# Performance work log

Measured on AMD Instinct MI355X. Metric: run time of the kernel, lower is better.

## Reference

```python
import jax, jax.numpy as jnp
import numpy as np

B, C, M, H, W = 4, 12, 2, 320, 320
TOL = 1e-6
MAX_ITER = 10


def to_c(t):
    # [..., 2] real -> complex
    return jax.lax.complex(t[..., 0], t[..., 1])


def to_r(t):
    return jnp.stack([jnp.real(t), jnp.imag(t)], axis=-1)


def fft2c(x):
    return jnp.fft.fft2(x, axes=(-2, -1), norm='ortho')


def ifft2c(x):
    return jnp.fft.ifft2(x, axes=(-2, -1), norm='ortho')


def A_op(x, sm, mk):
    # x: [B,M,H,W] complex, sm: [B,C,M,H,W] complex, mk: [B,C,H,W] real
    coil_imgs = jnp.sum(x[:, None] * sm, axis=2)  # [B,C,H,W]
    return fft2c(coil_imgs) * mk


def AT_op(y, sm, mk):
    img = ifft2c(y * mk)  # [B,C,H,W]
    return jnp.sum(jnp.conj(sm) * img[:, :, None], axis=1)  # [B,M,H,W]


def cg_solve(x0, Mop, tol=TOL, max_iter=MAX_ITER):
    b = x0.shape[0]
    x0x0 = jnp.sum(jnp.abs(x0.reshape(b, -1)) ** 2, axis=-1)  # [B] real

    def body(carry, _):
        x, r, p, rr = carry
        active = jnp.min(rr / x0x0) > tol  # tol check, gated like the while-loop
        q = Mop(p)
        pq = jnp.sum((p * jnp.conj(q)).reshape(b, -1), axis=-1)  # complexDot(p, q)
        alpha = rr.astype(x0.dtype) / pq  # complex_div(rr, <p,q>)
        a = alpha[:, None, None, None]
        x_new = x + a * p
        r_new = r - a * q
        rr_new = jnp.sum(jnp.abs(r_new.reshape(b, -1)) ** 2, axis=-1)
        beta = (rr_new / rr)[:, None, None, None].astype(x0.dtype)
        p_new = r_new + beta * p
        new = (x_new, r_new, p_new, rr_new)
        carry = jax.tree.map(lambda n, o: jnp.where(active, n, o), new, carry)
        return carry, None

    rr0 = jnp.sum(jnp.abs(x0.reshape(b, -1)) ** 2, axis=-1)
    init = (jnp.zeros_like(x0), x0, x0, rr0)
    (x, _, _, _), _ = jax.lax.scan(body, init, None, length=max_iter)
    return x


def setup_inputs() -> dict:
    key = jax.random.key(0)
    k1, k2, k3, k4 = jax.random.split(key, 4)
    x = jax.random.normal(k1, (B, M, H, W, 2), dtype=jnp.float32)
    y = jax.random.normal(k2, (B, C, H, W, 2), dtype=jnp.float32)
    smaps = jax.random.normal(k3, (B, C, M, H, W, 2), dtype=jnp.float32) * 0.2
    mask = jax.random.randint(k4, (B, C, H, W, 1), 0, 2).astype(jnp.float32)
    lambda_a = jnp.full((1,), 0.05, dtype=jnp.float32)
    return {"x": x, "y": y, "smaps": smaps, "mask": mask, "lambda_a": lambda_a}


def reference(x, y, smaps, mask, lambda_a):
    z = to_c(x)          # [B,M,H,W]
    yc = to_c(y)         # [B,C,H,W]
    sm = to_c(smaps)     # [B,C,M,H,W]
    mk = mask[..., 0]    # [B,C,H,W]
    lam = lambda_a[0]

    x0 = lam * AT_op(yc, sm, mk) + z

    def Mop(p):
        return lam * AT_op(A_op(p, sm, mk), sm, mk) + p

    return to_r(cg_solve(x0, Mop))
```

## Files before the change

kernel.cpp:

```cpp
#include <hip/hip_runtime.h>
#include <math.h>

#define NB 4
#define NC 12
#define NM 2
#define NN 320
#define NHW (NN*NN)
#define NBC (NB*NC)
#define CG_TOL 1e-6f
#define NITER 10
#define CBLK 400

#define TWO_PI_F 6.28318530717958647692f

typedef float2 c32;

__device__ __forceinline__ c32 cmul(c32 a, c32 b){ return make_float2(a.x*b.x - a.y*b.y, a.x*b.y + a.y*b.x); }
__device__ __forceinline__ c32 cmulj(c32 a, c32 b){ return make_float2(a.x*b.x + a.y*b.y, a.x*b.y - a.y*b.x); }
__device__ __forceinline__ c32 cadd(c32 a, c32 b){ return make_float2(a.x+b.x, a.y+b.y); }
__device__ __forceinline__ c32 csub(c32 a, c32 b){ return make_float2(a.x-b.x, a.y-b.y); }
__device__ __forceinline__ c32 cscale(c32 a, float s){ return make_float2(a.x*s, a.y*s); }

__device__ __forceinline__ float wave_reduce_f(float v) {
  #pragma unroll
  for (int off = 32; off >= 1; off >>= 1) v += __shfl_xor(v, off, 64);
  return v;
}
__device__ __forceinline__ c32 wave_reduce_c(c32 v) {
  #pragma unroll
  for (int off = 32; off >= 1; off >>= 1) {
    v.x += __shfl_xor(v.x, off, 64);
    v.y += __shfl_xor(v.y, off, 64);
  }
  return v;
}

__global__ __launch_bounds__(256)
void twiddle_init(c32* __restrict__ T320, c32* __restrict__ T64)
{
  const int t = threadIdx.x;
  {
    float s, c; sincosf(TWO_PI_F * (float)t / 320.f, &s, &c);
    T320[t] = make_float2(c, s);
  }
  if (t < 32) {
    float s, c; sincosf(TWO_PI_F * (float)t / 64.f, &s, &c);
    T64[t] = make_float2(c, s);
  }
}

template<int DIR>
__device__ __forceinline__ void fft320_tw(c32 A[5], const c32 ct[4], const c32 tw[6], int lane)
{
  constexpr float C72  = 0.30901699437494745f, S72  = 0.9510565162951535f;
  constexpr float C144 = -0.8090169943749475f, S144 = 0.5877852522924731f;
  const float sgn = (float)DIR;
  const c32 w51 = make_float2(C72,  sgn*S72);
  const c32 w52 = make_float2(C144, sgn*S144);
  const c32 w53 = make_float2(C144, -sgn*S144);
  const c32 w54 = make_float2(C72,  -sgn*S72);
  c32 v0=A[0], v1=A[1], v2=A[2], v3=A[3], v4=A[4];
  A[0] = cadd(cadd(v0, v1), cadd(cadd(v2, v3), v4));
  A[1] = cadd(v0, cadd(cadd(cmul(v1,w51), cmul(v2,w52)), cadd(cmul(v3,w53), cmul(v4,w54))));
  A[2] = cadd(v0, cadd(cadd(cmul(v1,w52), cmul(v2,w54)), cadd(cmul(v3,w51), cmul(v4,w53))));
  A[3] = cadd(v0, cadd(cadd(cmul(v1,w53), cmul(v2,w51)), cadd(cmul(v3,w54), cmul(v4,w52))));
  A[4] = cadd(v0, cadd(cadd(cmul(v1,w54), cmul(v2,w53)), cadd(cmul(v3,w52), cmul(v4,w51))));
  A[1] = cmul(A[1], ct[0]);
  A[2] = cmul(A[2], ct[1]);
  A[3] = cmul(A[3], ct[2]);
  A[4] = cmul(A[4], ct[3]);
  #pragma unroll
  for (int s = 0; s < 6; ++s) {
    const int m = 32 >> s;
    const c32 w = tw[s];
    const bool up = (lane & m) != 0;
    #pragma unroll
    for (int k1 = 0; k1 < 5; ++k1) {
      c32 o;
      o.x = __shfl_xor(A[k1].x, m, 64);
      o.y = __shfl_xor(A[k1].y, m, 64);
      c32 lo = cadd(A[k1], o);
      c32 hi = cmul(csub(o, A[k1]), w);
      A[k1] = up ? hi : lo;
    }
  }
}

template<int DIR, int IN_MODE, int OUT_MODE>
__global__ __launch_bounds__(256)
void fft_pass(const c32* __restrict__ in, c32* __restrict__ out,
              const c32* __restrict__ pvec, const c32* __restrict__ smaps,
              const float* __restrict__ mask, const float* __restrict__ flag,
              const c32* __restrict__ T320, const c32* __restrict__ T64)
{
  if (flag != nullptr && flag[0] == 0.f) return;
  __shared__ c32 tile[8][NN + 2];
  const int tid  = threadIdx.x;
  const int lane = tid & 63;
  const int wv   = tid >> 6;
  const int bc   = blockIdx.y;
  const int r0   = blockIdx.x * 8;
  const float sgn = (float)DIR;

  c32 ct[4], tw[6];
  #pragma unroll
  for (int k = 0; k < 4; ++k) {
    c32 t = T320[(k + 1) * lane];
    ct[k] = make_float2(t.x, sgn * t.y);
  }
  #pragma unroll
  for (int s = 0; s < 6; ++s) {
    const int m = 32 >> s;
    c32 t = T64[(lane & (m - 1)) << s];
    tw[s] = make_float2(t.x, sgn * t.y);
  }
  const int rv6 = __brev((unsigned)lane) >> 26;

  #pragma unroll
  for (int rep = 0; rep < 2; ++rep) {
    const int ri  = wv * 2 + rep;
    const int row = r0 + ri;
    c32 A[5];
    if constexpr (IN_MODE == 0) {
      #pragma unroll
      for (int j = 0; j < 5; ++j)
        A[j] = in[((size_t)bc * NN + row) * NN + lane + 64*j];
    } else if constexpr (IN_MODE == 1) {
      const int b = bc / NC;
      const int c = bc % NC;
      #pragma unroll
      for (int j = 0; j < 5; ++j) {
        const int col = lane + 64*j;
        const size_t hw = (size_t)row * NN + col;
        c32 p0 = pvec[(size_t)(b*NM + 0) * NHW + hw];
        c32 p1 = pvec[(size_t)(b*NM + 1) * NHW + hw];
        c32 s0 = smaps[(size_t)((b*NC + c)*NM + 0) * NHW + hw];
        c32 s1 = smaps[(size_t)((b*NC + c)*NM + 1) * NHW + hw];
        A[j] = cadd(cmul(p0, s0), cmul(p1, s1));
      }
    } else {
      #pragma unroll
      for (int j = 0; j < 5; ++j) {
        const size_t idx = ((size_t)bc * NN + row) * NN + lane + 64*j;
        A[j] = cscale(in[idx], mask[idx]);
      }
    }
    fft320_tw<DIR>(A, ct, tw, lane);
    #pragma unroll
    for (int k1 = 0; k1 < 5; ++k1)
      tile[ri][k1 + 5*rv6] = A[k1];
  }
  __syncthreads();
  if constexpr (OUT_MODE != 2) {
    #pragma unroll
    for (int it = 0; it < 10; ++it) {
      const int idx = it * 256 + tid;
      const int u = idx >> 3;
      const int d = idx & 7;
      c32 val = tile[d][u];
      const size_t oidx = ((size_t)bc * NN + u) * NN + (r0 + d);
      if constexpr (OUT_MODE == 1) val = cscale(val, mask[oidx]);
      out[oidx] = val;
    }
  } else {
    #pragma unroll
    for (int it = 0; it < 10; ++it) {
      const int idx = it * 256 + tid;
      const int d = idx / NN;
      const int u = idx - d * NN;
      out[((size_t)bc * NN + (r0 + d)) * NN + u] = tile[d][u];
    }
  }
}

__global__ __launch_bounds__(256)
void fft_mask_ifft(const c32* __restrict__ in, c32* __restrict__ out,
                   const float* __restrict__ mask, const float* __restrict__ flag,
                   const c32* __restrict__ T320, const c32* __restrict__ T64)
{
  if (flag[0] == 0.f) return;
  __shared__ c32 tile[8][NN + 2];
  const int tid  = threadIdx.x;
  const int lane = tid & 63;
  const int wv   = tid >> 6;
  const int bc   = blockIdx.y;
  const int r0   = blockIdx.x * 8;

  c32 ctf[4], twf[6], cti[4], twi[6];
  #pragma unroll
  for (int k = 0; k < 4; ++k) {
    c32 t = T320[(k + 1) * lane];
    ctf[k] = make_float2(t.x, -t.y);
    cti[k] = make_float2(t.x,  t.y);
  }
  #pragma unroll
  for (int s = 0; s < 6; ++s) {
    const int m = 32 >> s;
    c32 t = T64[(lane & (m - 1)) << s];
    twf[s] = make_float2(t.x, -t.y);
    twi[s] = make_float2(t.x,  t.y);
  }
  const int rv6 = __brev((unsigned)lane) >> 26;

  #pragma unroll
  for (int rep = 0; rep < 2; ++rep) {
    const int ri  = wv * 2 + rep;
    const int row = r0 + ri;
    c32 A[5];
    #pragma unroll
    for (int j = 0; j < 5; ++j)
      A[j] = in[((size_t)bc * NN + row) * NN + lane + 64*j];
    fft320_tw<-1>(A, ctf, twf, lane);
    #pragma unroll
    for (int k1 = 0; k1 < 5; ++k1) {
      const int kh = k1 + 5*rv6;
      A[k1] = cscale(A[k1], mask[(size_t)bc * NHW + (size_t)kh * NN + row]);
    }
    #pragma unroll
    for (int k1 = 0; k1 < 5; ++k1)
      tile[ri][k1 + 5*rv6] = A[k1];
    c32 Bv[5];
    #pragma unroll
    for (int j = 0; j < 5; ++j)
      Bv[j] = tile[ri][lane + 64*j];
    fft320_tw<1>(Bv, cti, twi, lane);
    #pragma unroll
    for (int k1 = 0; k1 < 5; ++k1)
      tile[ri][k1 + 5*rv6] = Bv[k1];
  }
  __syncthreads();
  #pragma unroll
  for (int it = 0; it < 10; ++it) {
    const int idx = it * 256 + tid;
    const int u = idx >> 3;
    const int d = idx & 7;
    out[((size_t)bc * NN + u) * NN + (r0 + d)] = tile[d][u];
  }
}

__global__ __launch_bounds__(256)
void init_combine(const c32* __restrict__ img, const c32* __restrict__ smaps,
                  const c32* __restrict__ z, c32* __restrict__ x,
                  c32* __restrict__ r, c32* __restrict__ p,
                  const float* __restrict__ lam, float* __restrict__ part)
{
  const int b  = blockIdx.y;
  const int hw = blockIdx.x * 256 + threadIdx.x;
  const float l0 = lam[0] * (1.f / (float)NN);
  c32 a0 = make_float2(0.f,0.f), a1 = make_float2(0.f,0.f);
  #pragma unroll
  for (int c = 0; c < NC; ++c) {
    c32 iv = img[(size_t)(b*NC + c) * NHW + hw];
    c32 s0 = smaps[(size_t)((b*NC + c)*NM + 0) * NHW + hw];
    c32 s1 = smaps[(size_t)((b*NC + c)*NM + 1) * NHW + hw];
    a0 = cadd(a0, cmulj(s0, iv));
    a1 = cadd(a1, cmulj(s1, iv));
  }
  const size_t i0 = (size_t)(b*NM + 0) * NHW + hw;
  const size_t i1 = (size_t)(b*NM + 1) * NHW + hw;
  c32 x00 = cadd(cscale(a0, l0), z[i0]);
  c32 x01 = cadd(cscale(a1, l0), z[i1]);
  x[i0] = make_float2(0.f,0.f); x[i1] = make_float2(0.f,0.f);
  r[i0] = x00; r[i1] = x01;
  p[i0] = x00; p[i1] = x01;
  float acc = x00.x*x00.x + x00.y*x00.y + x01.x*x01.x + x01.y*x01.y;
  acc = wave_reduce_f(acc);
  __shared__ float sred[4];
  const int lane = threadIdx.x & 63, wv = threadIdx.x >> 6;
  if (lane == 0) sred[wv] = acc;
  __syncthreads();
  if (threadIdx.x == 0) part[b*CBLK + blockIdx.x] = sred[0]+sred[1]+sred[2]+sred[3];
}

__global__ void reduce_init(const float* __restrict__ part, float* __restrict__ x0x0,
                            float* __restrict__ rr0, float* __restrict__ flags)
{
  const int lane = threadIdx.x & 63;
  const int b = threadIdx.x >> 6;
  float s = 0.f;
  for (int j = lane; j < CBLK; j += 64) s += part[b*CBLK + j];
  s = wave_reduce_f(s);
  if (lane == 0) { x0x0[b] = s; rr0[b] = s; }
  if (threadIdx.x == 0) flags[0] = 1.f;
}

__global__ __launch_bounds__(256)
void q_combine(const c32* __restrict__ img, const c32* __restrict__ smaps,
               const c32* __restrict__ p, c32* __restrict__ q,
               const float* __restrict__ lam, const float* __restrict__ flag,
               c32* __restrict__ pqpart)
{
  if (flag[0] == 0.f) return;
  const int b  = blockIdx.y;
  const int hw = blockIdx.x * 256 + threadIdx.x;
  const float lq = lam[0] * (1.f / (float)NHW);
  c32 a0 = make_float2(0.f,0.f), a1 = make_float2(0.f,0.f);
  #pragma unroll
  for (int c = 0; c < NC; ++c) {
    c32 iv = img[(size_t)(b*NC + c) * NHW + hw];
    c32 s0 = smaps[(size_t)((b*NC + c)*NM + 0) * NHW + hw];
    c32 s1 = smaps[(size_t)((b*NC + c)*NM + 1) * NHW + hw];
    a0 = cadd(a0, cmulj(s0, iv));
    a1 = cadd(a1, cmulj(s1, iv));
  }
  const size_t i0 = (size_t)(b*NM + 0) * NHW + hw;
  const size_t i1 = (size_t)(b*NM + 1) * NHW + hw;
  c32 p0 = p[i0], p1 = p[i1];
  c32 q0 = cadd(cscale(a0, lq), p0);
  c32 q1 = cadd(cscale(a1, lq), p1);
  q[i0] = q0; q[i1] = q1;
  c32 s = cadd(cmulj(q0, p0), cmulj(q1, p1));
  s = wave_reduce_c(s);
  __shared__ c32 sred[4];
  const int lane = threadIdx.x & 63, wv = threadIdx.x >> 6;
  if (lane == 0) sred[wv] = s;
  __syncthreads();
  if (threadIdx.x == 0)
    pqpart[b*CBLK + blockIdx.x] = cadd(cadd(sred[0], sred[1]), cadd(sred[2], sred[3]));
}

__global__ void reduce_pq(const c32* __restrict__ pqpart, c32* __restrict__ pqout,
                          const float* __restrict__ flag)
{
  if (flag[0] == 0.f) return;
  const int lane = threadIdx.x & 63;
  const int b = threadIdx.x >> 6;
  c32 s = make_float2(0.f, 0.f);
  for (int j = lane; j < CBLK; j += 64) s = cadd(s, pqpart[b*CBLK + j]);
  s = wave_reduce_c(s);
  if (lane == 0) pqout[b] = s;
}

__global__ __launch_bounds__(256)
void update1(c32* __restrict__ x, c32* __restrict__ r,
             const c32* __restrict__ p, const c32* __restrict__ q,
             const float* __restrict__ rr_i, const c32* __restrict__ pq_i,
             const float* __restrict__ flag, float* __restrict__ part)
{
  if (flag[0] == 0.f) return;
  const int b  = blockIdx.y;
  const int hw = blockIdx.x * 256 + threadIdx.x;
  const float rrv = rr_i[b];
  const c32 pqv = pq_i[b];
  const float den = pqv.x*pqv.x + pqv.y*pqv.y;
  const c32 alpha = make_float2(rrv * pqv.x / den, -rrv * pqv.y / den);
  float acc = 0.f;
  #pragma unroll
  for (int m = 0; m < NM; ++m) {
    const size_t idx = (size_t)(b*NM + m) * NHW + hw;
    c32 pe = p[idx], qe = q[idx];
    c32 xe = cadd(x[idx], cmul(alpha, pe));
    c32 re = csub(r[idx], cmul(alpha, qe));
    x[idx] = xe; r[idx] = re;
    acc += re.x*re.x + re.y*re.y;
  }
  acc = wave_reduce_f(acc);
  __shared__ float sred[4];
  const int lane = threadIdx.x & 63, wv = threadIdx.x >> 6;
  if (lane == 0) sred[wv] = acc;
  __syncthreads();
  if (threadIdx.x == 0) part[b*CBLK + blockIdx.x] = sred[0]+sred[1]+sred[2]+sred[3];
}

__global__ void reduce_rr(const float* __restrict__ part, const float* __restrict__ rr_i,
                          float* __restrict__ rr_n, const float* __restrict__ x0x0,
                          const float* __restrict__ flag_i, float* __restrict__ flag_n)
{
  const int lane = threadIdx.x & 63;
  const int b = threadIdx.x >> 6;
  __shared__ float sred[4];
  __shared__ float sx0[4];
  if (flag_i[0] == 0.f) {
    if (lane == 0) rr_n[b] = rr_i[b];
    if (threadIdx.x == 0) flag_n[0] = 0.f;
    return;
  }
  float s = 0.f;
  for (int j = lane; j < CBLK; j += 64) s += part[b*CBLK + j];
  s = wave_reduce_f(s);
  if (lane == 0) { rr_n[b] = s; sred[b] = s; sx0[b] = x0x0[b]; }
  __syncthreads();
  if (threadIdx.x == 0) {
    float mn = 1e30f;
    #pragma unroll
    for (int bb = 0; bb < NB; ++bb) mn = fminf(mn, sred[bb] / sx0[bb]);
    flag_n[0] = (mn > CG_TOL) ? 1.f : 0.f;
  }
}

__global__ __launch_bounds__(256)
void update2(c32* __restrict__ p, const c32* __restrict__ r,
             const float* __restrict__ rr_i, const float* __restrict__ rr_n,
             const float* __restrict__ flag)
{
  if (flag[0] == 0.f) return;
  const int b  = blockIdx.y;
  const int hw = blockIdx.x * 256 + threadIdx.x;
  const float beta = rr_n[b] / rr_i[b];
  #pragma unroll
  for (int m = 0; m < NM; ++m) {
    const size_t idx = (size_t)(b*NM + m) * NHW + hw;
    p[idx] = cadd(r[idx], cscale(p[idx], beta));
  }
}

extern "C" void kernel_launch(void* const* d_in, const int* in_sizes, int n_in,
                              void* d_out, int out_size, void* d_ws, size_t ws_size,
                              hipStream_t stream)
{
  const c32*  z   = (const c32*)d_in[0];
  const c32*  y   = (const c32*)d_in[1];
  const c32*  sm  = (const c32*)d_in[2];
  const float* mk = (const float*)d_in[3];
  const float* lam= (const float*)d_in[4];
  c32* x = (c32*)d_out;

  char* base = (char*)d_ws;
  size_t off = 0;
  auto walloc = [&](size_t bytes) -> void* {
    void* ptr = base + off;
    off += (bytes + 255) & ~(size_t)255;
    return ptr;
  };
  c32* buf1   = (c32*)walloc((size_t)NBC * NHW * sizeof(c32));
  c32* buf2   = (c32*)walloc((size_t)NBC * NHW * sizeof(c32));
  c32* rv     = (c32*)walloc((size_t)NB * NM * NHW * sizeof(c32));
  c32* pv     = (c32*)walloc((size_t)NB * NM * NHW * sizeof(c32));
  c32* qv     = (c32*)walloc((size_t)NB * NM * NHW * sizeof(c32));
  c32* pqpart = (c32*)walloc((size_t)NB * CBLK * sizeof(c32));
  c32* pq     = (c32*)walloc((size_t)NITER * NB * sizeof(c32));
  float* x0x0 = (float*)walloc(NB * sizeof(float));
  float* rr   = (float*)walloc((NITER + 1) * NB * sizeof(float));
  float* flags= (float*)walloc((NITER + 1) * sizeof(float));
  float* part1= (float*)walloc((size_t)NB * CBLK * sizeof(float));
  c32* T320   = (c32*)walloc(256 * sizeof(c32));
  c32* T64    = (c32*)walloc(32 * sizeof(c32));
  (void)ws_size; (void)in_sizes; (void)n_in; (void)out_size;

  dim3 fgrid(NN / 8, NBC), blk(256);
  dim3 cgrid(CBLK, NB);

  twiddle_init<<<1, 256, 0, stream>>>(T320, T64);

  fft_pass<1, 2, 0><<<fgrid, blk, 0, stream>>>(y,    buf2, nullptr, nullptr, mk,      nullptr, T320, T64);
  fft_pass<1, 0, 0><<<fgrid, blk, 0, stream>>>(buf2, buf1, nullptr, nullptr, nullptr, nullptr, T320, T64);
  init_combine<<<cgrid, blk, 0, stream>>>(buf1, sm, z, x, rv, pv, lam, part1);
  reduce_init<<<1, 256, 0, stream>>>(part1, x0x0, rr, flags);

  for (int i = 0; i < NITER; ++i) {
    const float* fl = flags + i;
    fft_pass<-1, 1, 0><<<fgrid, blk, 0, stream>>>(nullptr, buf2, pv, sm, nullptr, fl, T320, T64);
    fft_mask_ifft<<<fgrid, blk, 0, stream>>>(buf2, buf1, mk, fl, T320, T64);
    fft_pass<1, 0, 2><<<fgrid, blk, 0, stream>>>(buf1, buf2, nullptr, nullptr, nullptr, fl, T320, T64);
    q_combine<<<cgrid, blk, 0, stream>>>(buf2, sm, pv, qv, lam, fl, pqpart);
    reduce_pq<<<1, 256, 0, stream>>>(pqpart, pq + i*NB, fl);
    update1<<<cgrid, blk, 0, stream>>>(x, rv, pv, qv, rr + i*NB, pq + i*NB, fl, part1);
    reduce_rr<<<1, 256, 0, stream>>>(part1, rr + i*NB, rr + (i+1)*NB, x0x0, fl, flags + (i+1));
    update2<<<cgrid, blk, 0, stream>>>(pv, rv, rr + i*NB, rr + (i+1)*NB, fl);
  }
}
```

Baseline: 430.8 us.

## Fuse p-update into first FFT pass, fold pq reduction, batch two-row FFTs

```diff
diff --git a/kernel.cpp b/kernel.cpp
--- a/kernel.cpp
+++ b/kernel.cpp
@@ -21,6 +21,12 @@
 __device__ __forceinline__ c32 csub(c32 a, c32 b){ return make_float2(a.x-b.x, a.y-b.y); }
 __device__ __forceinline__ c32 cscale(c32 a, float s){ return make_float2(a.x*s, a.y*s); }
 
+template<bool FWD>
+__device__ __forceinline__ c32 twmul(c32 a, c32 t){
+  return FWD ? make_float2(a.x*t.x + a.y*t.y, a.y*t.x - a.x*t.y)
+             : make_float2(a.x*t.x - a.y*t.y, a.y*t.x + a.x*t.y);
+}
+
 __device__ __forceinline__ float wave_reduce_f(float v) {
   #pragma unroll
   for (int off = 32; off >= 1; off >>= 1) v += __shfl_xor(v, off, 64);
@@ -49,127 +55,160 @@
   }
 }
 
-template<int DIR>
-__device__ __forceinline__ void fft320_tw(c32 A[5], const c32 ct[4], const c32 tw[6], int lane)
-{
-  constexpr float C72  = 0.30901699437494745f, S72  = 0.9510565162951535f;
-  constexpr float C144 = -0.8090169943749475f, S144 = 0.5877852522924731f;
-  const float sgn = (float)DIR;
-  const c32 w51 = make_float2(C72,  sgn*S72);
-  const c32 w52 = make_float2(C144, sgn*S144);
-  const c32 w53 = make_float2(C144, -sgn*S144);
-  const c32 w54 = make_float2(C72,  -sgn*S72);
-  c32 v0=A[0], v1=A[1], v2=A[2], v3=A[3], v4=A[4];
-  A[0] = cadd(cadd(v0, v1), cadd(cadd(v2, v3), v4));
-  A[1] = cadd(v0, cadd(cadd(cmul(v1,w51), cmul(v2,w52)), cadd(cmul(v3,w53), cmul(v4,w54))));
-  A[2] = cadd(v0, cadd(cadd(cmul(v1,w52), cmul(v2,w54)), cadd(cmul(v3,w51), cmul(v4,w53))));
-  A[3] = cadd(v0, cadd(cadd(cmul(v1,w53), cmul(v2,w51)), cadd(cmul(v3,w54), cmul(v4,w52))));
-  A[4] = cadd(v0, cadd(cadd(cmul(v1,w54), cmul(v2,w53)), cadd(cmul(v3,w52), cmul(v4,w51))));
-  A[1] = cmul(A[1], ct[0]);
-  A[2] = cmul(A[2], ct[1]);
-  A[3] = cmul(A[3], ct[2]);
-  A[4] = cmul(A[4], ct[3]);
+template<bool FWD>
+__device__ __forceinline__ void radix5(c32 V[5]) {
+  constexpr float C1 = 0.30901699437494745f;
+  constexpr float S1 = 0.9510565162951535f;
+  constexpr float C2 = -0.8090169943749475f;
+  constexpr float S2 = 0.5877852522924731f;
+  constexpr float sg = FWD ? -1.f : 1.f;
+  const c32 w1 = make_float2(C1,  sg*S1);
+  const c32 w2 = make_float2(C2,  sg*S2);
+  const c32 w3 = make_float2(C2, -sg*S2);
+  const c32 w4 = make_float2(C1, -sg*S1);
+  c32 v0=V[0], v1=V[1], v2=V[2], v3=V[3], v4=V[4];
+  V[0] = cadd(cadd(v0, v1), cadd(cadd(v2, v3), v4));
+  V[1] = cadd(v0, cadd(cadd(cmul(v1,w1), cmul(v2,w2)), cadd(cmul(v3,w3), cmul(v4,w4))));
+  V[2] = cadd(v0, cadd(cadd(cmul(v1,w2), cmul(v2,w4)), cadd(cmul(v3,w1), cmul(v4,w3))));
+  V[3] = cadd(v0, cadd(cadd(cmul(v1,w3), cmul(v2,w1)), cadd(cmul(v3,w4), cmul(v4,w2))));
+  V[4] = cadd(v0, cadd(cadd(cmul(v1,w4), cmul(v2,w3)), cadd(cmul(v3,w2), cmul(v4,w1))));
+}
+
+template<bool FWD>
+__device__ __forceinline__ void fft320_x2(c32 A[5], c32 B[5],
+                                          const c32 ct[4], const c32 tw[6], int lane)
+{
+  radix5<FWD>(A);
+  radix5<FWD>(B);
+  #pragma unroll
+  for (int k = 1; k < 5; ++k) {
+    A[k] = twmul<FWD>(A[k], ct[k-1]);
+    B[k] = twmul<FWD>(B[k], ct[k-1]);
+  }
   #pragma unroll
   for (int s = 0; s < 6; ++s) {
     const int m = 32 >> s;
     const c32 w = tw[s];
     const bool up = (lane & m) != 0;
-    #pragma unroll
-    for (int k1 = 0; k1 < 5; ++k1) {
-      c32 o;
-      o.x = __shfl_xor(A[k1].x, m, 64);
-      o.y = __shfl_xor(A[k1].y, m, 64);
-      c32 lo = cadd(A[k1], o);
-      c32 hi = cmul(csub(o, A[k1]), w);
-      A[k1] = up ? hi : lo;
+    c32 oA[5], oB[5];
+    #pragma unroll
+    for (int k = 0; k < 5; ++k) { oA[k].x = __shfl_xor(A[k].x, m, 64); oA[k].y = __shfl_xor(A[k].y, m, 64); }
+    #pragma unroll
+    for (int k = 0; k < 5; ++k) { oB[k].x = __shfl_xor(B[k].x, m, 64); oB[k].y = __shfl_xor(B[k].y, m, 64); }
+    #pragma unroll
+    for (int k = 0; k < 5; ++k) {
+      c32 loA = cadd(A[k], oA[k]);
+      c32 hiA = twmul<FWD>(csub(oA[k], A[k]), w);
+      A[k] = up ? hiA : loA;
+      c32 loB = cadd(B[k], oB[k]);
+      c32 hiB = twmul<FWD>(csub(oB[k], B[k]), w);
+      B[k] = up ? hiB : loB;
     }
   }
 }
 
-template<int DIR, int IN_MODE, int OUT_MODE>
+#define LOAD_TWIDDLES \
+  c32 ct[4], tw[6]; \
+  _Pragma("unroll") for (int k_ = 0; k_ < 4; ++k_) ct[k_] = T320[(k_ + 1) * lane]; \
+  _Pragma("unroll") for (int s_ = 0; s_ < 6; ++s_) tw[s_] = T64[(lane & ((32 >> s_) - 1)) << s_];
+
+template<bool FWD, bool MASK_IN, bool NAT_OUT>
 __global__ __launch_bounds__(256)
 void fft_pass(const c32* __restrict__ in, c32* __restrict__ out,
-              const c32* __restrict__ pvec, const c32* __restrict__ smaps,
               const float* __restrict__ mask, const float* __restrict__ flag,
               const c32* __restrict__ T320, const c32* __restrict__ T64)
 {
   if (flag != nullptr && flag[0] == 0.f) return;
   __shared__ c32 tile[8][NN + 2];
-  const int tid  = threadIdx.x;
-  const int lane = tid & 63;
-  const int wv   = tid >> 6;
-  const int bc   = blockIdx.y;
-  const int r0   = blockIdx.x * 8;
-  const float sgn = (float)DIR;
-
-  c32 ct[4], tw[6];
-  #pragma unroll
-  for (int k = 0; k < 4; ++k) {
-    c32 t = T320[(k + 1) * lane];
-    ct[k] = make_float2(t.x, sgn * t.y);
-  }
-  #pragma unroll
-  for (int s = 0; s < 6; ++s) {
-    const int m = 32 >> s;
-    c32 t = T64[(lane & (m - 1)) << s];
-    tw[s] = make_float2(t.x, sgn * t.y);
-  }
+  const int tid = threadIdx.x, lane = tid & 63, wv = tid >> 6;
+  const int bc = blockIdx.y, r0 = blockIdx.x * 8;
+  LOAD_TWIDDLES
   const int rv6 = __brev((unsigned)lane) >> 26;
-
-  #pragma unroll
-  for (int rep = 0; rep < 2; ++rep) {
-    const int ri  = wv * 2 + rep;
-    const int row = r0 + ri;
-    c32 A[5];
-    if constexpr (IN_MODE == 0) {
-      #pragma unroll
-      for (int j = 0; j < 5; ++j)
-        A[j] = in[((size_t)bc * NN + row) * NN + lane + 64*j];
-    } else if constexpr (IN_MODE == 1) {
-      const int b = bc / NC;
-      const int c = bc % NC;
-      #pragma unroll
-      for (int j = 0; j < 5; ++j) {
-        const int col = lane + 64*j;
-        const size_t hw = (size_t)row * NN + col;
-        c32 p0 = pvec[(size_t)(b*NM + 0) * NHW + hw];
-        c32 p1 = pvec[(size_t)(b*NM + 1) * NHW + hw];
-        c32 s0 = smaps[(size_t)((b*NC + c)*NM + 0) * NHW + hw];
-        c32 s1 = smaps[(size_t)((b*NC + c)*NM + 1) * NHW + hw];
-        A[j] = cadd(cmul(p0, s0), cmul(p1, s1));
+  const int rA = r0 + wv*2, rB = rA + 1;
+  c32 A[5], B[5];
+  #pragma unroll
+  for (int j = 0; j < 5; ++j) {
+    const size_t iA = ((size_t)bc * NN + rA) * NN + lane + 64*j;
+    const size_t iB = ((size_t)bc * NN + rB) * NN + lane + 64*j;
+    A[j] = in[iA]; B[j] = in[iB];
+    if constexpr (MASK_IN) { A[j] = cscale(A[j], mask[iA]); B[j] = cscale(B[j], mask[iB]); }
+  }
+  fft320_x2<FWD>(A, B, ct, tw, lane);
+  #pragma unroll
+  for (int k = 0; k < 5; ++k) {
+    tile[wv*2    ][k + 5*rv6] = A[k];
+    tile[wv*2 + 1][k + 5*rv6] = B[k];
+  }
+  __syncthreads();
+  if constexpr (!NAT_OUT) {
+    #pragma unroll
+    for (int it = 0; it < 10; ++it) {
+      const int idx = it * 256 + tid, u = idx >> 3, d = idx & 7;
+      out[((size_t)bc * NN + u) * NN + (r0 + d)] = tile[d][u];
+    }
+  } else {
+    #pragma unroll
+    for (int it = 0; it < 10; ++it) {
+      const int idx = it * 256 + tid, d = idx / NN, u = idx - d * NN;
+      out[((size_t)bc * NN + (r0 + d)) * NN + u] = tile[d][u];
+    }
+  }
+}
+
+__global__ __launch_bounds__(256)
+void fft_comb(c32* __restrict__ out, const c32* __restrict__ pin,
+              const c32* __restrict__ rres, c32* __restrict__ pout,
+              const c32* __restrict__ smaps,
+              const float* __restrict__ rr_prev, const float* __restrict__ rr_cur,
+              const float* __restrict__ flag,
+              const c32* __restrict__ T320, const c32* __restrict__ T64)
+{
+  if (flag[0] == 0.f) return;
+  __shared__ c32 tile[8][NN + 2];
+  const int tid = threadIdx.x, lane = tid & 63, wv = tid >> 6;
+  const int bc = blockIdx.y, r0 = blockIdx.x * 8;
+  const int b = bc / NC, c = bc - b * NC;
+  const bool upd = (rr_cur != nullptr);
+  const float beta = upd ? rr_cur[b] / rr_prev[b] : 0.f;
+  LOAD_TWIDDLES
+  const int rv6 = __brev((unsigned)lane) >> 26;
+  const int rA = r0 + wv*2, rB = rA + 1;
+  const size_t m0 = (size_t)(b*NM + 0) * NHW, m1 = (size_t)(b*NM + 1) * NHW;
+  const size_t s0o = (size_t)((b*NC + c)*NM + 0) * NHW, s1o = (size_t)((b*NC + c)*NM + 1) * NHW;
+  c32 A[5], B[5];
+  #pragma unroll
+  for (int j = 0; j < 5; ++j) {
+    const size_t hA = (size_t)rA * NN + lane + 64*j;
+    const size_t hB = (size_t)rB * NN + lane + 64*j;
+    c32 r0A = rres[m0 + hA], r1A = rres[m1 + hA];
+    c32 r0B = rres[m0 + hB], r1B = rres[m1 + hB];
+    c32 p0A, p1A, p0B, p1B;
+    if (upd) {
+      p0A = cadd(r0A, cscale(pin[m0 + hA], beta));
+      p1A = cadd(r1A, cscale(pin[m1 + hA], beta));
+      p0B = cadd(r0B, cscale(pin[m0 + hB], beta));
+      p1B = cadd(r1B, cscale(pin[m1 + hB], beta));
+      if (c == 0) {
+        pout[m0 + hA] = p0A; pout[m1 + hA] = p1A;
+        pout[m0 + hB] = p0B; pout[m1 + hB] = p1B;
       }
     } else {
-      #pragma unroll
-      for (int j = 0; j < 5; ++j) {
-        const size_t idx = ((size_t)bc * NN + row) * NN + lane + 64*j;
-        A[j] = cscale(in[idx], mask[idx]);
-      }
+      p0A = r0A; p1A = r1A; p0B = r0B; p1B = r1B;
     }
-    fft320_tw<DIR>(A, ct, tw, lane);
-    #pragma unroll
-    for (int k1 = 0; k1 < 5; ++k1)
-      tile[ri][k1 + 5*rv6] = A[k1];
-  }
-  __syncthreads();
-  if constexpr (OUT_MODE != 2) {
-    #pragma unroll
-    for (int it = 0; it < 10; ++it) {
-      const int idx = it * 256 + tid;
-      const int u = idx >> 3;
-      const int d = idx & 7;
-      c32 val = tile[d][u];
-      const size_t oidx = ((size_t)bc * NN + u) * NN + (r0 + d);
-      if constexpr (OUT_MODE == 1) val = cscale(val, mask[oidx]);
-      out[oidx] = val;
-    }
-  } else {
-    #pragma unroll
-    for (int it = 0; it < 10; ++it) {
-      const int idx = it * 256 + tid;
-      const int d = idx / NN;
-      const int u = idx - d * NN;
-      out[((size_t)bc * NN + (r0 + d)) * NN + u] = tile[d][u];
-    }
+    A[j] = cadd(cmul(p0A, smaps[s0o + hA]), cmul(p1A, smaps[s1o + hA]));
+    B[j] = cadd(cmul(p0B, smaps[s0o + hB]), cmul(p1B, smaps[s1o + hB]));
+  }
+  fft320_x2<true>(A, B, ct, tw, lane);
+  #pragma unroll
+  for (int k = 0; k < 5; ++k) {
+    tile[wv*2    ][k + 5*rv6] = A[k];
+    tile[wv*2 + 1][k + 5*rv6] = B[k];
+  }
+  __syncthreads();
+  #pragma unroll
+  for (int it = 0; it < 10; ++it) {
+    const int idx = it * 256 + tid, u = idx >> 3, d = idx & 7;
+    out[((size_t)bc * NN + u) * NN + (r0 + d)] = tile[d][u];
   }
 }
 
@@ -180,60 +219,44 @@
 {
   if (flag[0] == 0.f) return;
   __shared__ c32 tile[8][NN + 2];
-  const int tid  = threadIdx.x;
-  const int lane = tid & 63;
-  const int wv   = tid >> 6;
-  const int bc   = blockIdx.y;
-  const int r0   = blockIdx.x * 8;
-
-  c32 ctf[4], twf[6], cti[4], twi[6];
-  #pragma unroll
-  for (int k = 0; k < 4; ++k) {
-    c32 t = T320[(k + 1) * lane];
-    ctf[k] = make_float2(t.x, -t.y);
-    cti[k] = make_float2(t.x,  t.y);
-  }
-  #pragma unroll
-  for (int s = 0; s < 6; ++s) {
-    const int m = 32 >> s;
-    c32 t = T64[(lane & (m - 1)) << s];
-    twf[s] = make_float2(t.x, -t.y);
-    twi[s] = make_float2(t.x,  t.y);
-  }
+  const int tid = threadIdx.x, lane = tid & 63, wv = tid >> 6;
+  const int bc = blockIdx.y, r0 = blockIdx.x * 8;
+  LOAD_TWIDDLES
   const int rv6 = __brev((unsigned)lane) >> 26;
-
-  #pragma unroll
-  for (int rep = 0; rep < 2; ++rep) {
-    const int ri  = wv * 2 + rep;
-    const int row = r0 + ri;
-    c32 A[5];
-    #pragma unroll
-    for (int j = 0; j < 5; ++j)
-      A[j] = in[((size_t)bc * NN + row) * NN + lane + 64*j];
-    fft320_tw<-1>(A, ctf, twf, lane);
-    #pragma unroll
-    for (int k1 = 0; k1 < 5; ++k1) {
-      const int kh = k1 + 5*rv6;
-      A[k1] = cscale(A[k1], mask[(size_t)bc * NHW + (size_t)kh * NN + row]);
-    }
-    #pragma unroll
-    for (int k1 = 0; k1 < 5; ++k1)
-      tile[ri][k1 + 5*rv6] = A[k1];
-    c32 Bv[5];
-    #pragma unroll
-    for (int j = 0; j < 5; ++j)
-      Bv[j] = tile[ri][lane + 64*j];
-    fft320_tw<1>(Bv, cti, twi, lane);
-    #pragma unroll
-    for (int k1 = 0; k1 < 5; ++k1)
-      tile[ri][k1 + 5*rv6] = Bv[k1];
+  const int rA = r0 + wv*2, rB = rA + 1;
+  c32 A[5], B[5];
+  #pragma unroll
+  for (int j = 0; j < 5; ++j) {
+    A[j] = in[((size_t)bc * NN + rA) * NN + lane + 64*j];
+    B[j] = in[((size_t)bc * NN + rB) * NN + lane + 64*j];
+  }
+  fft320_x2<true>(A, B, ct, tw, lane);
+  #pragma unroll
+  for (int k = 0; k < 5; ++k) {
+    const int kh = k + 5*rv6;
+    A[k] = cscale(A[k], mask[(size_t)bc * NHW + (size_t)kh * NN + rA]);
+    B[k] = cscale(B[k], mask[(size_t)bc * NHW + (size_t)kh * NN + rB]);
+  }
+  #pragma unroll
+  for (int k = 0; k < 5; ++k) {
+    tile[wv*2    ][k + 5*rv6] = A[k];
+    tile[wv*2 + 1][k + 5*rv6] = B[k];
+  }
+  #pragma unroll
+  for (int j = 0; j < 5; ++j) {
+    A[j] = tile[wv*2    ][lane + 64*j];
+    B[j] = tile[wv*2 + 1][lane + 64*j];
+  }
+  fft320_x2<false>(A, B, ct, tw, lane);
+  #pragma unroll
+  for (int k = 0; k < 5; ++k) {
+    tile[wv*2    ][k + 5*rv6] = A[k];
+    tile[wv*2 + 1][k + 5*rv6] = B[k];
   }
   __syncthreads();
   #pragma unroll
   for (int it = 0; it < 10; ++it) {
-    const int idx = it * 256 + tid;
-    const int u = idx >> 3;
-    const int d = idx & 7;
+    const int idx = it * 256 + tid, u = idx >> 3, d = idx & 7;
     out[((size_t)bc * NN + u) * NN + (r0 + d)] = tile[d][u];
   }
 }
@@ -319,31 +342,27 @@
     pqpart[b*CBLK + blockIdx.x] = cadd(cadd(sred[0], sred[1]), cadd(sred[2], sred[3]));
 }
 
-__global__ void reduce_pq(const c32* __restrict__ pqpart, c32* __restrict__ pqout,
-                          const float* __restrict__ flag)
-{
-  if (flag[0] == 0.f) return;
-  const int lane = threadIdx.x & 63;
-  const int b = threadIdx.x >> 6;
-  c32 s = make_float2(0.f, 0.f);
-  for (int j = lane; j < CBLK; j += 64) s = cadd(s, pqpart[b*CBLK + j]);
-  s = wave_reduce_c(s);
-  if (lane == 0) pqout[b] = s;
-}
-
 __global__ __launch_bounds__(256)
 void update1(c32* __restrict__ x, c32* __restrict__ r,
              const c32* __restrict__ p, const c32* __restrict__ q,
-             const float* __restrict__ rr_i, const c32* __restrict__ pq_i,
+             const float* __restrict__ rr_i, const c32* __restrict__ pqpart,
              const float* __restrict__ flag, float* __restrict__ part)
 {
   if (flag[0] == 0.f) return;
-  const int b  = blockIdx.y;
-  const int hw = blockIdx.x * 256 + threadIdx.x;
+  const int b = blockIdx.y;
+  const int t = threadIdx.x;
+  c32 s = make_float2(0.f, 0.f);
+  for (int j = t; j < CBLK; j += 256) s = cadd(s, pqpart[b*CBLK + j]);
+  s = wave_reduce_c(s);
+  __shared__ c32 spq[4];
+  const int lane = t & 63, wv = t >> 6;
+  if (lane == 0) spq[wv] = s;
+  __syncthreads();
+  const c32 pqv = cadd(cadd(spq[0], spq[1]), cadd(spq[2], spq[3]));
   const float rrv = rr_i[b];
-  const c32 pqv = pq_i[b];
   const float den = pqv.x*pqv.x + pqv.y*pqv.y;
   const c32 alpha = make_float2(rrv * pqv.x / den, -rrv * pqv.y / den);
+  const int hw = blockIdx.x * 256 + t;
   float acc = 0.f;
   #pragma unroll
   for (int m = 0; m < NM; ++m) {
@@ -356,10 +375,9 @@
   }
   acc = wave_reduce_f(acc);
   __shared__ float sred[4];
-  const int lane = threadIdx.x & 63, wv = threadIdx.x >> 6;
   if (lane == 0) sred[wv] = acc;
   __syncthreads();
-  if (threadIdx.x == 0) part[b*CBLK + blockIdx.x] = sred[0]+sred[1]+sred[2]+sred[3];
+  if (t == 0) part[b*CBLK + blockIdx.x] = sred[0]+sred[1]+sred[2]+sred[3];
 }
 
 __global__ void reduce_rr(const float* __restrict__ part, const float* __restrict__ rr_i,
@@ -385,22 +403,6 @@
     #pragma unroll
     for (int bb = 0; bb < NB; ++bb) mn = fminf(mn, sred[bb] / sx0[bb]);
     flag_n[0] = (mn > CG_TOL) ? 1.f : 0.f;
-  }
-}
-
-__global__ __launch_bounds__(256)
-void update2(c32* __restrict__ p, const c32* __restrict__ r,
-             const float* __restrict__ rr_i, const float* __restrict__ rr_n,
-             const float* __restrict__ flag)
-{
-  if (flag[0] == 0.f) return;
-  const int b  = blockIdx.y;
-  const int hw = blockIdx.x * 256 + threadIdx.x;
-  const float beta = rr_n[b] / rr_i[b];
-  #pragma unroll
-  for (int m = 0; m < NM; ++m) {
-    const size_t idx = (size_t)(b*NM + m) * NHW + hw;
-    p[idx] = cadd(r[idx], cscale(p[idx], beta));
   }
 }
 
@@ -425,10 +427,10 @@
   c32* buf1   = (c32*)walloc((size_t)NBC * NHW * sizeof(c32));
   c32* buf2   = (c32*)walloc((size_t)NBC * NHW * sizeof(c32));
   c32* rv     = (c32*)walloc((size_t)NB * NM * NHW * sizeof(c32));
-  c32* pv     = (c32*)walloc((size_t)NB * NM * NHW * sizeof(c32));
+  c32* pvA    = (c32*)walloc((size_t)NB * NM * NHW * sizeof(c32));
+  c32* pvB    = (c32*)walloc((size_t)NB * NM * NHW * sizeof(c32));
   c32* qv     = (c32*)walloc((size_t)NB * NM * NHW * sizeof(c32));
   c32* pqpart = (c32*)walloc((size_t)NB * CBLK * sizeof(c32));
-  c32* pq     = (c32*)walloc((size_t)NITER * NB * sizeof(c32));
   float* x0x0 = (float*)walloc(NB * sizeof(float));
   float* rr   = (float*)walloc((NITER + 1) * NB * sizeof(float));
   float* flags= (float*)walloc((NITER + 1) * sizeof(float));
@@ -442,20 +444,22 @@
 
   twiddle_init<<<1, 256, 0, stream>>>(T320, T64);
 
-  fft_pass<1, 2, 0><<<fgrid, blk, 0, stream>>>(y,    buf2, nullptr, nullptr, mk,      nullptr, T320, T64);
-  fft_pass<1, 0, 0><<<fgrid, blk, 0, stream>>>(buf2, buf1, nullptr, nullptr, nullptr, nullptr, T320, T64);
-  init_combine<<<cgrid, blk, 0, stream>>>(buf1, sm, z, x, rv, pv, lam, part1);
+  fft_pass<false, true,  false><<<fgrid, blk, 0, stream>>>(y,    buf2, mk,      nullptr, T320, T64);
+  fft_pass<false, false, false><<<fgrid, blk, 0, stream>>>(buf2, buf1, nullptr, nullptr, T320, T64);
+  init_combine<<<cgrid, blk, 0, stream>>>(buf1, sm, z, x, rv, pvA, lam, part1);
   reduce_init<<<1, 256, 0, stream>>>(part1, x0x0, rr, flags);
 
   for (int i = 0; i < NITER; ++i) {
     const float* fl = flags + i;
-    fft_pass<-1, 1, 0><<<fgrid, blk, 0, stream>>>(nullptr, buf2, pv, sm, nullptr, fl, T320, T64);
+    c32* pin  = (i & 1) ? pvA : pvB;
+    c32* pout = (i & 1) ? pvB : pvA;
+    const float* rrprev = (i > 0) ? (rr + (i-1)*NB) : rr;
+    const float* rrcur  = (i > 0) ? (rr + i*NB) : nullptr;
+    fft_comb<<<fgrid, blk, 0, stream>>>(buf2, pin, rv, pout, sm, rrprev, rrcur, fl, T320, T64);
     fft_mask_ifft<<<fgrid, blk, 0, stream>>>(buf2, buf1, mk, fl, T320, T64);
-    fft_pass<1, 0, 2><<<fgrid, blk, 0, stream>>>(buf1, buf2, nullptr, nullptr, nullptr, fl, T320, T64);
-    q_combine<<<cgrid, blk, 0, stream>>>(buf2, sm, pv, qv, lam, fl, pqpart);
-    reduce_pq<<<1, 256, 0, stream>>>(pqpart, pq + i*NB, fl);
-    update1<<<cgrid, blk, 0, stream>>>(x, rv, pv, qv, rr + i*NB, pq + i*NB, fl, part1);
+    fft_pass<false, false, true><<<fgrid, blk, 0, stream>>>(buf1, buf2, nullptr, fl, T320, T64);
+    q_combine<<<cgrid, blk, 0, stream>>>(buf2, sm, pout, qv, lam, fl, pqpart);
+    update1<<<cgrid, blk, 0, stream>>>(x, rv, pout, qv, rr + i*NB, pqpart, fl, part1);
     reduce_rr<<<1, 256, 0, stream>>>(part1, rr + i*NB, rr + (i+1)*NB, x0x0, fl, flags + (i+1));
-    update2<<<cgrid, blk, 0, stream>>>(pv, rv, rr + i*NB, rr + (i+1)*NB, fl);
-  }
-}
+  }
+}
```

After: 398.9 us. 1.08x faster.
